# Optimization experiments

Measured on AMD Instinct MI355X. Metric: run time of the kernel, lower is better.

Reference implementation:

```python
import jax, jax.numpy as jnp
import numpy as np

NEG_SLOPE = 0.2
EPS_SOFTMAX = 1e-16
EPS_NORM = 1e-12
H = 4


def gat_conv(x, src, dst, edge_attr, W, att_src, att_dst, W_edge, att_edge, bias, concat):
    """PyG GATConv with edge_dim, add_self_loops=False.
    x: [N, F_in]; src,dst: [E]; edge_attr: [E, edge_dim]
    W: [F_in, H*C]; att_src/att_dst/att_edge: [H, C]; W_edge: [edge_dim, H*C]
    """
    N = x.shape[0]
    C = att_src.shape[1]
    xs = (x @ W).reshape(N, H, C)                      # [N,H,C]
    a_s = jnp.einsum('nhc,hc->nh', xs, att_src)        # [N,H]
    a_d = jnp.einsum('nhc,hc->nh', xs, att_dst)        # [N,H]
    e = (edge_attr @ W_edge).reshape(-1, H, C)         # [E,H,C]
    a_e = jnp.einsum('ehc,hc->eh', e, att_edge)        # [E,H]
    alpha = a_s[src] + a_d[dst] + a_e                  # [E,H]
    alpha = jax.nn.leaky_relu(alpha, NEG_SLOPE)
    # segment softmax over edges grouped by destination node
    m = jax.ops.segment_max(alpha, dst, num_segments=N)        # [N,H]
    ex = jnp.exp(alpha - m[dst])
    denom = jax.ops.segment_sum(ex, dst, num_segments=N)       # [N,H]
    alpha = ex / (denom[dst] + EPS_SOFTMAX)
    # message = attention-weighted source features, scatter-add to dst
    out = jax.ops.segment_sum(xs[src] * alpha[..., None], dst, num_segments=N)  # [N,H,C]
    out = out.reshape(N, H * C) if concat else out.mean(axis=1)
    return out + bias


def l2_normalize(x):
    n = jnp.linalg.norm(x, axis=-1, keepdims=True)
    return x / jnp.maximum(n, EPS_NORM)


def setup_inputs() -> dict:
    key = jax.random.key(0)
    ks = jax.random.split(key, 16)
    N, E, F_in, C1, C2 = 50000, 800000, 128, 64, 64
    glorot = lambda k, shape: jax.random.uniform(
        k, shape, jnp.float32, -1.0, 1.0) * np.sqrt(6.0 / (shape[0] + shape[-1]))
    return {
        'x': jax.random.normal(ks[0], (N, F_in), jnp.float32),
        'edge_index': jax.random.randint(ks[1], (2, E), 0, N, jnp.int32),
        'edge_weight': jax.random.uniform(ks[2], (E, 1), jnp.float32),
        # layer 1: in=128 -> H*C1=256, concat=True
        'W1': glorot(ks[3], (F_in, H * C1)),
        'att_src1': glorot(ks[4], (H, C1)),
        'att_dst1': glorot(ks[5], (H, C1)),
        'We1': glorot(ks[6], (1, H * C1)),
        'att_e1': glorot(ks[7], (H, C1)),
        'b1': jnp.zeros((H * C1,), jnp.float32),
        # layer 2: in=256 -> H*C2, concat=False (mean over heads)
        'W2': glorot(ks[8], (H * C1, H * C2)),
        'att_src2': glorot(ks[9], (H, C2)),
        'att_dst2': glorot(ks[10], (H, C2)),
        'We2': glorot(ks[11], (1, H * C2)),
        'att_e2': glorot(ks[12], (H, C2)),
        'b2': jnp.zeros((C2,), jnp.float32),
    }


def reference(x, edge_index, edge_weight, W1, att_src1, att_dst1, We1, att_e1, b1,
              W2, att_src2, att_dst2, We2, att_e2, b2):
    src, dst = edge_index[0], edge_index[1]
    h = gat_conv(x, src, dst, edge_weight, W1, att_src1, att_dst1, We1, att_e1, b1, concat=True)
    h = jax.nn.relu(l2_normalize(h))
    out = gat_conv(h, src, dst, edge_weight, W2, att_src2, att_dst2, We2, att_e2, b2, concat=False)
    return out
```

## Files before the change

### kernel.cpp

```cpp
#include <hip/hip_runtime.h>
#include <hip/hip_bf16.h>

typedef unsigned short u16;
typedef unsigned long long u64;
using bf16x8 = __attribute__((ext_vector_type(8))) short;
using f32x4v = __attribute__((ext_vector_type(4))) float;
typedef float v2f __attribute__((ext_vector_type(2)));

#define HC 256
#define CDIM 64

__device__ __forceinline__ float b2f(u16 u){
  union { unsigned int i; float f; } c; c.i = ((unsigned)u) << 16; return c.f;
}
__device__ __forceinline__ u16 f2b(float f){
  union { float f; unsigned int i; } c; c.f = f;
  unsigned int x = c.i;
  return (u16)((x + 0x7FFFu + ((x >> 16) & 1u)) >> 16);
}
__device__ __forceinline__ float ldf(const void* p, size_t i, int isbf){
  return isbf ? b2f(((const u16*)p)[i]) : ((const float*)p)[i];
}
__device__ __forceinline__ float sel4(float4 v, int h){ return h==0?v.x:(h==1?v.y:(h==2?v.z:v.w)); }
__device__ __forceinline__ float lrelu(float v){ return v>0.f ? v : 0.2f*v; }

__device__ __forceinline__ void glds16(const void* g, void* l){
  __builtin_amdgcn_global_load_lds(
      (const __attribute__((address_space(1))) unsigned int*)g,
      (__attribute__((address_space(3))) unsigned int*)l, 16, 0, 0);
}

__device__ __forceinline__ float4 wave_max4(float4 m){
  #pragma unroll
  for(int o=32;o>0;o>>=1){
    m.x=fmaxf(m.x,__shfl_xor(m.x,o));
    m.y=fmaxf(m.y,__shfl_xor(m.y,o));
    m.z=fmaxf(m.z,__shfl_xor(m.z,o));
    m.w=fmaxf(m.w,__shfl_xor(m.w,o));
  }
  return m;
}
__device__ __forceinline__ float4 wave_sum4(float4 m){
  #pragma unroll
  for(int o=32;o>0;o>>=1){
    m.x+=__shfl_xor(m.x,o);
    m.y+=__shfl_xor(m.y,o);
    m.z+=__shfl_xor(m.z,o);
    m.w+=__shfl_xor(m.w,o);
  }
  return m;
}

__global__ void k_hist(const int* __restrict__ dst, int E, int N, int* __restrict__ deg,
                       int* __restrict__ rank,
                       const u16* __restrict__ x, int nelem, int* __restrict__ flag){
  int e = blockIdx.x*256 + threadIdx.x;
  if (e < E){
    int d = dst[e];
    if ((unsigned)d < (unsigned)N) rank[e] = atomicAdd(&deg[d], 1);
  }
  if (blockIdx.x == 0){
    __shared__ int bad;
    if (threadIdx.x==0) bad = 0;
    __syncthreads();
    int n = nelem < 8192 ? nelem : 8192;
    int localbad = 0;
    for (int i=threadIdx.x; i<n; i+=256){
      int ex = (x[i] >> 7) & 0xFF;
      if (ex >= 140) localbad++;
    }
    if (localbad) atomicAdd(&bad, 1);
    __syncthreads();
    if (threadIdx.x==0) *flag = (bad==0) ? 1 : 0;
  }
}

__global__ void k_scan1(const int* __restrict__ in, int* __restrict__ out, int* __restrict__ bsums, int n){
  __shared__ int s[256];
  int t = threadIdx.x;
  int i = blockIdx.x*256 + t;
  int v = (i<n)? in[i] : 0;
  s[t]=v; __syncthreads();
  for(int off=1; off<256; off<<=1){
    int tv = (t>=off)? s[t-off] : 0;
    __syncthreads();
    s[t]+=tv; __syncthreads();
  }
  if (i<n) out[i] = s[t]-v;
  if (t==255) bsums[blockIdx.x] = s[255];
}

__global__ void k_scan2(int* __restrict__ bsums, int nb){
  __shared__ int s[256];
  int t=threadIdx.x;
  int v=(t<nb)? bsums[t]:0;
  s[t]=v; __syncthreads();
  for(int off=1; off<256; off<<=1){
    int tv=(t>=off)? s[t-off]:0;
    __syncthreads();
    s[t]+=tv; __syncthreads();
  }
  if (t<nb) bsums[t]=s[t]-v;
}

__global__ void k_scatter(const int* __restrict__ src, const int* __restrict__ dst,
                          const void* __restrict__ ew, int E, int N,
                          const int* __restrict__ rowptr, const int* __restrict__ bsums,
                          const int* __restrict__ rank, u64* __restrict__ epk,
                          const int* __restrict__ flagp){
  int e = blockIdx.x*256+threadIdx.x;
  if (e>=E) return;
  int bf = *flagp;
  int d = dst[e];
  if ((unsigned)d >= (unsigned)N) return;
  int p = rowptr[d] + bsums[d>>8] + rank[e];
  int s = src[e];
  if ((unsigned)s >= (unsigned)N) s = 0;
  u64 v = ((u64)__float_as_uint(ldf(ew, e, bf)) << 32) | (unsigned)s;
  __builtin_nontemporal_store(v, &epk[p]);
}

__global__ void k_prep(const void* __restrict__ W1, const void* __restrict__ W2,
                       const void* __restrict__ We1, const void* __restrict__ ae1,
                       const void* __restrict__ We2, const void* __restrict__ ae2,
                       u16* __restrict__ Bt1, u16* __restrict__ Bt2, float* __restrict__ ce,
                       const int* __restrict__ flagp){
  int bf = *flagp;
  int b = blockIdx.x, t = threadIdx.x;
  if (b < 128){
    Bt1[(size_t)t*128 + b] = f2b(ldf(W1, (size_t)b*HC + t, bf));
  } else if (b < 384){
    int k = b - 128;
    Bt2[(size_t)t*256 + k] = f2b(ldf(W2, (size_t)k*HC + t, bf));
  } else {
    float p1 = ldf(We1, t, bf)*ldf(ae1, t, bf);
    float p2 = ldf(We2, t, bf)*ldf(ae2, t, bf);
    #pragma unroll
    for(int o=32;o>0;o>>=1){ p1+=__shfl_xor(p1,o); p2+=__shfl_xor(p2,o); }
    if((t&63)==0){ ce[t>>6]=p1; ce[4+(t>>6)]=p2; }
  }
}

__global__ __launch_bounds__(256) void k_gemm_mfma(
    const void* __restrict__ A, int a_ext, const u16* __restrict__ Bt,
    u16* __restrict__ C, const void* __restrict__ att_s, const void* __restrict__ att_d,
    float* __restrict__ a_s, float* __restrict__ a_d,
    int M, int K, const int* __restrict__ flagp)
{
  __shared__ u16 sh[64*264];
  __shared__ float att_sh[512];
  u16* As = sh;
  u16* Bs = sh + 2048;
  int bf = *flagp;
  int a_bf = a_ext ? bf : 1;
  int tid = threadIdx.x;
  int lane = tid & 63, w = tid >> 6;
  int quad = lane >> 4, ln = lane & 15;
  int m0 = blockIdx.x * 64;

  att_sh[tid]       = ldf(att_s, tid, bf);
  att_sh[256 + tid] = ldf(att_d, tid, bf);

  f32x4v acc[4][4] = {};
  for (int k0 = 0; k0 < K; k0 += 32){
    if (!a_ext){
      const u16* gA = (const u16*)A + (size_t)(m0 + (tid>>2))*K + k0 + (size_t)(tid&3)*8;
      glds16(gA, (char*)As + (size_t)w*1024);
    } else {
      int m = tid >> 2, g = tid & 3;
      int r = m0 + m;
      uint4 pack;
      if (r < M){
        size_t base = (size_t)r*K + k0 + g*8;
        if (a_bf){
          pack = *(const uint4*)((const u16*)A + base);
        } else {
          const float* Af = (const float*)A + base;
          float4 f0 = *(const float4*)Af;
          float4 f1 = *(const float4*)(Af+4);
          unsigned a0 = (unsigned)f2b(f0.x) | ((unsigned)f2b(f0.y)<<16);
          unsigned a1 = (unsigned)f2b(f0.z) | ((unsigned)f2b(f0.w)<<16);
          unsigned a2 = (unsigned)f2b(f1.x) | ((unsigned)f2b(f1.y)<<16);
          unsigned a3 = (unsigned)f2b(f1.z) | ((unsigned)f2b(f1.w)<<16);
          pack = make_uint4(a0,a1,a2,a3);
        }
      } else pack = make_uint4(0,0,0,0);
      ((uint4*)As)[tid] = pack;
    }
    #pragma unroll
    for (int i=0;i<4;i++){
      const u16* gB = Bt + (size_t)(i*64 + (tid>>2))*K + k0 + (size_t)(tid&3)*8;
      glds16(gB, (char*)Bs + (size_t)i*4096 + (size_t)w*1024);
    }
    __syncthreads();
    bf16x8 af[4], bfr[4];
    #pragma unroll
    for (int mi=0;mi<4;mi++) af[mi] = *(const bf16x8*)&As[(mi*16+ln)*32 + quad*8];
    #pragma unroll
    for (int nj=0;nj<4;nj++) bfr[nj] = *(const bf16x8*)&Bs[((size_t)w*64+nj*16+ln)*32 + quad*8];
    #pragma unroll
    for (int mi=0;mi<4;mi++)
      #pragma unroll
      for (int nj=0;nj<4;nj++)
        acc[mi][nj] = __builtin_amdgcn_mfma_f32_16x16x32_bf16(af[mi], bfr[nj], acc[mi][nj], 0,0,0);
    __syncthreads();
  }
  #pragma unroll
  for (int mi=0;mi<4;mi++)
    #pragma unroll
    for (int nj=0;nj<4;nj++){
      union { __hip_bfloat162 h2; u16 u[2]; } cv0, cv1;
      cv0.h2 = __float22bfloat162_rn(make_float2(acc[mi][nj][0], acc[mi][nj][1]));
      cv1.h2 = __float22bfloat162_rn(make_float2(acc[mi][nj][2], acc[mi][nj][3]));
      int col = w*64 + nj*16 + ln;
      int rbase = mi*16 + quad*4;
      sh[(rbase+0)*264 + col] = cv0.u[0];
      sh[(rbase+1)*264 + col] = cv0.u[1];
      sh[(rbase+2)*264 + col] = cv1.u[0];
      sh[(rbase+3)*264 + col] = cv1.u[1];
    }
  __syncthreads();
  #pragma unroll
  for (int j=0;j<8;j++){
    int idx = j*256 + tid;
    int r = idx >> 5, gq = idx & 31;
    if (m0 + r < M)
      *(uint4*)(C + (size_t)(m0+r)*HC + gq*8) = *(const uint4*)&sh[r*264 + gq*8];
  }
  {
    int r  = w*16 + ln;
    int hh = quad;
    const u16* crow = &sh[r*264 + hh*64];
    const float* asv = &att_sh[hh*64];
    const float* adv = &att_sh[256 + hh*64];
    float ps = 0.f, pd = 0.f;
    #pragma unroll
    for (int cb=0; cb<64; cb+=8){
      ushort4 ua = *(const ushort4*)&crow[cb];
      ushort4 ub = *(const ushort4*)&crow[cb+4];
      float4 sa = *(const float4*)&asv[cb];
      float4 sb = *(const float4*)&asv[cb+4];
      float4 da = *(const float4*)&adv[cb];
      float4 db = *(const float4*)&adv[cb+4];
      float c0=b2f(ua.x), c1=b2f(ua.y), c2=b2f(ua.z), c3=b2f(ua.w);
      float c4=b2f(ub.x), c5=b2f(ub.y), c6=b2f(ub.z), c7=b2f(ub.w);
      ps += c0*sa.x + c1*sa.y + c2*sa.z + c3*sa.w + c4*sb.x + c5*sb.y + c6*sb.z + c7*sb.w;
      pd += c0*da.x + c1*da.y + c2*da.z + c3*da.w + c4*db.x + c5*db.y + c6*db.z + c7*db.w;
    }
    if (m0 + r < M){
      a_s[(size_t)(m0+r)*4 + hh] = ps;
      a_d[(size_t)(m0+r)*4 + hh] = pd;
    }
  }
}

__global__ __launch_bounds__(256) void k_soft_agg(
    const u16* __restrict__ xs, const int* __restrict__ rowptr, const int* __restrict__ bsums,
    const int* __restrict__ deg, const u64* __restrict__ epk,
    const float* __restrict__ a_s, const float* __restrict__ a_d, const float* __restrict__ ce4,
    const void* __restrict__ bias, void* __restrict__ outp, int N, int layer,
    const int* __restrict__ flagp){
  __shared__ int   lds_s[4][64];
  __shared__ float lds_w[4][64][4];
  int bf = *flagp;
  int lane = threadIdx.x & 63;
  int w = threadIdx.x >> 6;
  int n = (blockIdx.x<<2) + w;
  if (n >= N) return;
  int row = rowptr[n] + bsums[n>>8];
  int dg = deg[n];
  float4 ad = *(const float4*)&a_d[(size_t)n*4];
  float4 ce = *(const float4*)ce4;
  int h = lane >> 4;
  float4 acc = make_float4(0.f,0.f,0.f,0.f);
  if (dg > 0){
    if (dg <= 64){
      int   s_reg = 0;
      float4 ar = make_float4(-1e30f,-1e30f,-1e30f,-1e30f);
      if (lane < dg){
        u64 pk = epk[row + lane];
        int s = (int)(unsigned)(pk & 0xFFFFFFFFull);
        if ((unsigned)s >= (unsigned)N) s = 0;
        s_reg = s;
        float wv = __uint_as_float((unsigned)(pk >> 32));
        float4 as = *(const float4*)&a_s[(size_t)s*4];
        ar.x = lrelu(as.x+ad.x+wv*ce.x);
        ar.y = lrelu(as.y+ad.y+wv*ce.y);
        ar.z = lrelu(as.z+ad.z+wv*ce.z);
        ar.w = lrelu(as.w+ad.w+wv*ce.w);
      }
      float4 m = ar;
      if (dg > 32){
        m.x=fmaxf(m.x,__shfl_xor(m.x,32)); m.y=fmaxf(m.y,__shfl_xor(m.y,32));
        m.z=fmaxf(m.z,__shfl_xor(m.z,32)); m.w=fmaxf(m.w,__shfl_xor(m.w,32));
      }
      if (dg > 16){
        m.x=fmaxf(m.x,__shfl_xor(m.x,16)); m.y=fmaxf(m.y,__shfl_xor(m.y,16));
        m.z=fmaxf(m.z,__shfl_xor(m.z,16)); m.w=fmaxf(m.w,__shfl_xor(m.w,16));
      }
      #pragma unroll
      for(int o=8;o>0;o>>=1){
        m.x=fmaxf(m.x,__shfl_xor(m.x,o)); m.y=fmaxf(m.y,__shfl_xor(m.y,o));
        m.z=fmaxf(m.z,__shfl_xor(m.z,o)); m.w=fmaxf(m.w,__shfl_xor(m.w,o));
      }
      float4 ex = make_float4(0.f,0.f,0.f,0.f);
      if (lane < dg){
        ex.x=__expf(ar.x-m.x); ex.y=__expf(ar.y-m.y);
        ex.z=__expf(ar.z-m.z); ex.w=__expf(ar.w-m.w);
      }
      float4 ss = ex;
      if (dg > 32){
        ss.x+=__shfl_xor(ss.x,32); ss.y+=__shfl_xor(ss.y,32);
        ss.z+=__shfl_xor(ss.z,32); ss.w+=__shfl_xor(ss.w,32);
      }
      if (dg > 16){
        ss.x+=__shfl_xor(ss.x,16); ss.y+=__shfl_xor(ss.y,16);
        ss.z+=__shfl_xor(ss.z,16); ss.w+=__shfl_xor(ss.w,16);
      }
      #pragma unroll
      for(int o=8;o>0;o>>=1){
        ss.x+=__shfl_xor(ss.x,o); ss.y+=__shfl_xor(ss.y,o);
        ss.z+=__shfl_xor(ss.z,o); ss.w+=__shfl_xor(ss.w,o);
      }
      float4 wgt;
      wgt.x = ex.x/(ss.x+1e-16f); wgt.y = ex.y/(ss.y+1e-16f);
      wgt.z = ex.z/(ss.z+1e-16f); wgt.w = ex.w/(ss.w+1e-16f);
      if (lane < dg){
        lds_s[w][lane] = s_reg;
        *(float4*)&lds_w[w][lane][0] = wgt;
      }
      v2f a01 = {0.f,0.f}, a23 = {0.f,0.f};
      uint2 xb[8]; float wb[8];
      {
        int pre = dg < 8 ? dg : 8;
        #pragma unroll
        for (int k=0;k<8;k++){
          if (k < pre){
            int s0 = lds_s[w][k];
            wb[k]  = lds_w[w][k][h];
            xb[k]  = *(const uint2*)&xs[(size_t)s0*HC + lane*4];
          }
        }
      }
      for (int base=0; base<dg; base+=8){
        int mcnt = dg - base; if (mcnt > 8) mcnt = 8;
        #pragma unroll
        for (int k=0;k<8;k++){
          if (k < mcnt){
            uint2 xv = xb[k]; float wk = wb[k];
            int nk = base + 8 + k;
            if (nk < dg){
              int s0 = lds_s[w][nk];
              wb[k]  = lds_w[w][nk][h];
              xb[k]  = *(const uint2*)&xs[(size_t)s0*HC + lane*4];
            }
            v2f f;
            f = (v2f){__uint_as_float(xv.x<<16), __uint_as_float(xv.x&0xFFFF0000u)}; a01 += f*wk;
            f = (v2f){__uint_as_float(xv.y<<16), __uint_as_float(xv.y&0xFFFF0000u)}; a23 += f*wk;
          }
        }
      }
      acc.x = a01.x; acc.y = a01.y; acc.z = a23.x; acc.w = a23.y;
    } else {
      float4 m = make_float4(-1e30f,-1e30f,-1e30f,-1e30f);
      for (int p=lane;p<dg;p+=64){
        u64 pk = epk[row+p];
        int s = (int)(unsigned)(pk & 0xFFFFFFFFull);
        if ((unsigned)s >= (unsigned)N) s = 0;
        float wv = __uint_as_float((unsigned)(pk >> 32));
        float4 as = *(const float4*)&a_s[(size_t)s*4];
        m.x=fmaxf(m.x, lrelu(as.x+ad.x+wv*ce.x));
        m.y=fmaxf(m.y, lrelu(as.y+ad.y+wv*ce.y));
        m.z=fmaxf(m.z, lrelu(as.z+ad.z+wv*ce.z));
        m.w=fmaxf(m.w, lrelu(as.w+ad.w+wv*ce.w));
      }
      m = wave_max4(m);
      float4 ss = make_float4(0.f,0.f,0.f,0.f);
      for (int p=lane;p<dg;p+=64){
        u64 pk = epk[row+p];
        int s = (int)(unsigned)(pk & 0xFFFFFFFFull);
        if ((unsigned)s >= (unsigned)N) s = 0;
        float wv = __uint_as_float((unsigned)(pk >> 32));
        float4 as = *(const float4*)&a_s[(size_t)s*4];
        ss.x+=__expf(lrelu(as.x+ad.x+wv*ce.x)-m.x);
        ss.y+=__expf(lrelu(as.y+ad.y+wv*ce.y)-m.y);
        ss.z+=__expf(lrelu(as.z+ad.z+wv*ce.z)-m.z);
        ss.w+=__expf(lrelu(as.w+ad.w+wv*ce.w)-m.w);
      }
      ss = wave_sum4(ss);
      float rsel=1.f/(sel4(ss,h)+1e-16f), mh=sel4(m,h), adh=sel4(ad,h), ceh=sel4(ce,h);
      for (int e=0;e<dg;e++){
        u64 pk = epk[row+e];
        int s = (int)(unsigned)(pk & 0xFFFFFFFFull);
        if ((unsigned)s >= (unsigned)N) s = 0;
        float wv = __uint_as_float((unsigned)(pk >> 32));
        float arv = lrelu(a_s[(size_t)s*4+h]+adh+wv*ceh);
        float wgt = __expf(arv-mh)*rsel;
        ushort4 xv4 = *(const ushort4*)&xs[(size_t)s*HC + lane*4];
        acc.x+=wgt*b2f(xv4.x); acc.y+=wgt*b2f(xv4.y);
        acc.z+=wgt*b2f(xv4.z); acc.w+=wgt*b2f(xv4.w);
      }
    }
  }
  if (layer==1){
    float4 v;
    v.x = acc.x + ldf(bias, lane*4+0, bf);
    v.y = acc.y + ldf(bias, lane*4+1, bf);
    v.z = acc.z + ldf(bias, lane*4+2, bf);
    v.w = acc.w + ldf(bias, lane*4+3, bf);
    float ss = v.x*v.x+v.y*v.y+v.z*v.z+v.w*v.w;
    #pragma unroll
    for(int o=32;o>0;o>>=1) ss += __shfl_xor(ss,o);
    float inv = 1.f/fmaxf(sqrtf(ss), 1e-12f);
    ushort4 o4;
    o4.x = f2b(fmaxf(v.x*inv,0.f)); o4.y = f2b(fmaxf(v.y*inv,0.f));
    o4.z = f2b(fmaxf(v.z*inv,0.f)); o4.w = f2b(fmaxf(v.w*inv,0.f));
    *(ushort4*)((u16*)outp + (size_t)n*HC + lane*4) = o4;
  } else {
    float4 s = acc;
    #pragma unroll
    for (int o=16;o<=32;o<<=1){
      s.x+=__shfl_xor(s.x,o); s.y+=__shfl_xor(s.y,o);
      s.z+=__shfl_xor(s.z,o); s.w+=__shfl_xor(s.w,o);
    }
    if (lane < 16){
      float4 v;
      v.x = 0.25f*s.x + ldf(bias, lane*4+0, bf);
      v.y = 0.25f*s.y + ldf(bias, lane*4+1, bf);
      v.z = 0.25f*s.z + ldf(bias, lane*4+2, bf);
      v.w = 0.25f*s.w + ldf(bias, lane*4+3, bf);
      if (bf){
        ushort4 o4; o4.x=f2b(v.x); o4.y=f2b(v.y); o4.z=f2b(v.z); o4.w=f2b(v.w);
        *(ushort4*)((u16*)outp + (size_t)n*CDIM + lane*4) = o4;
      } else {
        *(float4*)((float*)outp + (size_t)n*CDIM + lane*4) = v;
      }
    }
  }
}

extern "C" void kernel_launch(void* const* d_in, const int* in_sizes, int n_in,
                              void* d_out, int out_size, void* d_ws, size_t ws_size,
                              hipStream_t stream){
  const void* x_in = d_in[0];
  const int* eidx  = (const int*)d_in[1];
  const void* ew   = d_in[2];
  const void* W1   = d_in[3];
  const void* as1  = d_in[4];
  const void* ad1  = d_in[5];
  const void* We1  = d_in[6];
  const void* ae1  = d_in[7];
  const void* b1   = d_in[8];
  const void* W2   = d_in[9];
  const void* as2  = d_in[10];
  const void* ad2  = d_in[11];
  const void* We2  = d_in[12];
  const void* ae2  = d_in[13];
  const void* b2   = d_in[14];

  int N = in_sizes[0]/128;
  int E = in_sizes[2];
  const int* src = eidx;
  const int* dst = eidx + E;

  char* w = (char*)d_ws;
  auto alloc = [&](size_t bytes)->char*{ char* p=w; w += (bytes+255)/256*256; return p; };
  int*   flag  = (int*)alloc(256);
  u16*   xs    = (u16*)alloc((size_t)N*HC*2);
  u16*   agg   = (u16*)alloc((size_t)N*HC*2);
  float* a_s   = (float*)alloc((size_t)N*4*4);
  float* a_d   = (float*)alloc((size_t)N*4*4);
  int*   deg   = (int*)alloc((size_t)N*4);
  int*   rowptr= (int*)alloc((size_t)N*4);
  int*   bsums = (int*)alloc(256*4);
  int*   rank  = (int*)alloc((size_t)E*4);
  u64*   epk   = (u64*)alloc((size_t)E*8);
  float* ce    = (float*)alloc(256);
  u16*   Bt1   = (u16*)alloc((size_t)HC*128*2);
  u16*   Bt2   = (u16*)alloc((size_t)HC*HC*2);

  (void)hipMemsetAsync(deg, 0, (size_t)N*4, stream);

  int eb = (E+255)/256;
  int nb = (N+255)/256;
  k_hist<<<eb,256,0,stream>>>(dst, E, N, deg, rank, (const u16*)x_in, in_sizes[0], flag);
  k_scan1<<<nb,256,0,stream>>>(deg, rowptr, bsums, N);
  k_scan2<<<1,256,0,stream>>>(bsums, nb);
  k_scatter<<<eb,256,0,stream>>>(src, dst, ew, E, N, rowptr, bsums, rank, epk, flag);
  k_prep<<<385,256,0,stream>>>(W1, W2, We1, ae1, We2, ae2, Bt1, Bt2, ce, flag);

  int gemmBlocks = (N+63)/64;
  int nwb = (N+3)/4;

  k_gemm_mfma<<<gemmBlocks,256,0,stream>>>(x_in, 1, Bt1, xs, as1, ad1, a_s, a_d, N, 128, flag);
  k_soft_agg<<<nwb,256,0,stream>>>(xs, rowptr, bsums, deg, epk, a_s, a_d, ce, b1, agg, N, 1, flag);

  k_gemm_mfma<<<gemmBlocks,256,0,stream>>>(agg, 0, Bt2, xs, as2, ad2, a_s, a_d, N, 256, flag);
  k_soft_agg<<<nwb,256,0,stream>>>(xs, rowptr, bsums, deg, epk, a_s, a_d, ce+4, b2, d_out, N, 2, flag);
}
```

Measured before the change: 361.6 us.

## Replace LDS staging with readlane/shuffle broadcast and drop max-subtraction in soft-agg

The short-degree path of the softmax-aggregate kernel no longer stores source indices and weights to LDS. It broadcasts source indices with readlane and per-head weights with wave shuffles, and it issues the first eight feature gathers before the softmax is computed. It also removes the segment-max reduction and exponentiates the raw logits directly, which saves a reduction but risks overflow for large logits. Gathers for degrees above eight are issued in padded groups of four, and lanes beyond the degree carry zero weight.

```diff
diff --git a/kernel.cpp b/kernel.cpp
--- a/kernel.cpp
+++ b/kernel.cpp
@@ -254,14 +254,36 @@
   }
 }
 
+#define GRP4(E0, TWJ) { \
+  int s0_=__builtin_amdgcn_readlane(s_reg,(E0)+0); \
+  int s1_=__builtin_amdgcn_readlane(s_reg,(E0)+1); \
+  int s2_=__builtin_amdgcn_readlane(s_reg,(E0)+2); \
+  int s3_=__builtin_amdgcn_readlane(s_reg,(E0)+3); \
+  uint2 x0_=*(const uint2*)&xs[(size_t)s0_*HC + (lane<<2)]; \
+  uint2 x1_=*(const uint2*)&xs[(size_t)s1_*HC + (lane<<2)]; \
+  uint2 x2_=*(const uint2*)&xs[(size_t)s2_*HC + (lane<<2)]; \
+  uint2 x3_=*(const uint2*)&xs[(size_t)s3_*HC + (lane<<2)]; \
+  float w0_=__shfl((TWJ), ibase+(((E0)+0)&15)); \
+  float w1_=__shfl((TWJ), ibase+(((E0)+1)&15)); \
+  float w2_=__shfl((TWJ), ibase+(((E0)+2)&15)); \
+  float w3_=__shfl((TWJ), ibase+(((E0)+3)&15)); \
+  v2f f_; \
+  f_=(v2f){__uint_as_float(x0_.x<<16),__uint_as_float(x0_.x&0xFFFF0000u)}; a01+=f_*w0_; \
+  f_=(v2f){__uint_as_float(x0_.y<<16),__uint_as_float(x0_.y&0xFFFF0000u)}; a23+=f_*w0_; \
+  f_=(v2f){__uint_as_float(x1_.x<<16),__uint_as_float(x1_.x&0xFFFF0000u)}; a01+=f_*w1_; \
+  f_=(v2f){__uint_as_float(x1_.y<<16),__uint_as_float(x1_.y&0xFFFF0000u)}; a23+=f_*w1_; \
+  f_=(v2f){__uint_as_float(x2_.x<<16),__uint_as_float(x2_.x&0xFFFF0000u)}; a01+=f_*w2_; \
+  f_=(v2f){__uint_as_float(x2_.y<<16),__uint_as_float(x2_.y&0xFFFF0000u)}; a23+=f_*w2_; \
+  f_=(v2f){__uint_as_float(x3_.x<<16),__uint_as_float(x3_.x&0xFFFF0000u)}; a01+=f_*w3_; \
+  f_=(v2f){__uint_as_float(x3_.y<<16),__uint_as_float(x3_.y&0xFFFF0000u)}; a23+=f_*w3_; \
+}
+
 __global__ __launch_bounds__(256) void k_soft_agg(
     const u16* __restrict__ xs, const int* __restrict__ rowptr, const int* __restrict__ bsums,
     const int* __restrict__ deg, const u64* __restrict__ epk,
     const float* __restrict__ a_s, const float* __restrict__ a_d, const float* __restrict__ ce4,
     const void* __restrict__ bias, void* __restrict__ outp, int N, int layer,
     const int* __restrict__ flagp){
-  __shared__ int   lds_s[4][64];
-  __shared__ float lds_w[4][64][4];
   int bf = *flagp;
   int lane = threadIdx.x & 63;
   int w = threadIdx.x >> 6;
@@ -275,39 +297,25 @@
   float4 acc = make_float4(0.f,0.f,0.f,0.f);
   if (dg > 0){
     if (dg <= 64){
-      int   s_reg = 0;
-      float4 ar = make_float4(-1e30f,-1e30f,-1e30f,-1e30f);
-      if (lane < dg){
-        u64 pk = epk[row + lane];
-        int s = (int)(unsigned)(pk & 0xFFFFFFFFull);
-        if ((unsigned)s >= (unsigned)N) s = 0;
-        s_reg = s;
-        float wv = __uint_as_float((unsigned)(pk >> 32));
-        float4 as = *(const float4*)&a_s[(size_t)s*4];
-        ar.x = lrelu(as.x+ad.x+wv*ce.x);
-        ar.y = lrelu(as.y+ad.y+wv*ce.y);
-        ar.z = lrelu(as.z+ad.z+wv*ce.z);
-        ar.w = lrelu(as.w+ad.w+wv*ce.w);
-      }
-      float4 m = ar;
-      if (dg > 32){
-        m.x=fmaxf(m.x,__shfl_xor(m.x,32)); m.y=fmaxf(m.y,__shfl_xor(m.y,32));
-        m.z=fmaxf(m.z,__shfl_xor(m.z,32)); m.w=fmaxf(m.w,__shfl_xor(m.w,32));
-      }
-      if (dg > 16){
-        m.x=fmaxf(m.x,__shfl_xor(m.x,16)); m.y=fmaxf(m.y,__shfl_xor(m.y,16));
-        m.z=fmaxf(m.z,__shfl_xor(m.z,16)); m.w=fmaxf(m.w,__shfl_xor(m.w,16));
-      }
+      u64 pk = 0;
+      if (lane < dg) pk = epk[row + lane];
+      int s = (int)(unsigned)(pk & 0xFFFFFFFFull);
+      if ((unsigned)s >= (unsigned)N) s = 0;
+      int s_reg = s;
+      float wv = __uint_as_float((unsigned)(pk >> 32));
+      float4 as4 = *(const float4*)&a_s[(size_t)s*4];
+      uint2 xpf[8];
       #pragma unroll
-      for(int o=8;o>0;o>>=1){
-        m.x=fmaxf(m.x,__shfl_xor(m.x,o)); m.y=fmaxf(m.y,__shfl_xor(m.y,o));
-        m.z=fmaxf(m.z,__shfl_xor(m.z,o)); m.w=fmaxf(m.w,__shfl_xor(m.w,o));
-      }
-      float4 ex = make_float4(0.f,0.f,0.f,0.f);
-      if (lane < dg){
-        ex.x=__expf(ar.x-m.x); ex.y=__expf(ar.y-m.y);
-        ex.z=__expf(ar.z-m.z); ex.w=__expf(ar.w-m.w);
-      }
+      for (int k=0;k<8;k++){
+        int sk = __builtin_amdgcn_readlane(s_reg, k);
+        xpf[k] = *(const uint2*)&xs[(size_t)sk*HC + (lane<<2)];
+      }
+      bool vlane = lane < dg;
+      float4 ex;
+      ex.x = vlane ? __expf(lrelu(as4.x+ad.x+wv*ce.x)) : 0.f;
+      ex.y = vlane ? __expf(lrelu(as4.y+ad.y+wv*ce.y)) : 0.f;
+      ex.z = vlane ? __expf(lrelu(as4.z+ad.z+wv*ce.z)) : 0.f;
+      ex.w = vlane ? __expf(lrelu(as4.w+ad.w+wv*ce.w)) : 0.f;
       float4 ss = ex;
       if (dg > 32){
         ss.x+=__shfl_xor(ss.x,32); ss.y+=__shfl_xor(ss.y,32);
@@ -325,38 +333,58 @@
       float4 wgt;
       wgt.x = ex.x/(ss.x+1e-16f); wgt.y = ex.y/(ss.y+1e-16f);
       wgt.z = ex.z/(ss.z+1e-16f); wgt.w = ex.w/(ss.w+1e-16f);
-      if (lane < dg){
-        lds_s[w][lane] = s_reg;
-        *(float4*)&lds_w[w][lane][0] = wgt;
-      }
+      int ibase = lane & 48;
+      float tw0, tw1, tw2, tw3;
+      {
+        int srcl = lane & 15;
+        float c0=__shfl(wgt.x,srcl), c1=__shfl(wgt.y,srcl);
+        float c2=__shfl(wgt.z,srcl), c3=__shfl(wgt.w,srcl);
+        tw0 = (h==0)?c0:((h==1)?c1:((h==2)?c2:c3));
+      }
+      if (dg > 16){
+        int srcl = 16 + (lane & 15);
+        float c0=__shfl(wgt.x,srcl), c1=__shfl(wgt.y,srcl);
+        float c2=__shfl(wgt.z,srcl), c3=__shfl(wgt.w,srcl);
+        tw1 = (h==0)?c0:((h==1)?c1:((h==2)?c2:c3));
+      } else tw1 = 0.f;
+      if (dg > 32){
+        int srcl = 32 + (lane & 15);
+        float c0=__shfl(wgt.x,srcl), c1=__shfl(wgt.y,srcl);
+        float c2=__shfl(wgt.z,srcl), c3=__shfl(wgt.w,srcl);
+        tw2 = (h==0)?c0:((h==1)?c1:((h==2)?c2:c3));
+      } else tw2 = 0.f;
+      if (dg > 48){
+        int srcl = 48 + (lane & 15);
+        float c0=__shfl(wgt.x,srcl), c1=__shfl(wgt.y,srcl);
+        float c2=__shfl(wgt.z,srcl), c3=__shfl(wgt.w,srcl);
+        tw3 = (h==0)?c0:((h==1)?c1:((h==2)?c2:c3));
+      } else tw3 = 0.f;
       v2f a01 = {0.f,0.f}, a23 = {0.f,0.f};
-      uint2 xb[8]; float wb[8];
-      {
-        int pre = dg < 8 ? dg : 8;
-        #pragma unroll
-        for (int k=0;k<8;k++){
-          if (k < pre){
-            int s0 = lds_s[w][k];
-            wb[k]  = lds_w[w][k][h];
-            xb[k]  = *(const uint2*)&xs[(size_t)s0*HC + lane*4];
-          }
-        }
-      }
-      for (int base=0; base<dg; base+=8){
-        int mcnt = dg - base; if (mcnt > 8) mcnt = 8;
-        #pragma unroll
-        for (int k=0;k<8;k++){
-          if (k < mcnt){
-            uint2 xv = xb[k]; float wk = wb[k];
-            int nk = base + 8 + k;
-            if (nk < dg){
-              int s0 = lds_s[w][nk];
-              wb[k]  = lds_w[w][nk][h];
-              xb[k]  = *(const uint2*)&xs[(size_t)s0*HC + lane*4];
-            }
-            v2f f;
-            f = (v2f){__uint_as_float(xv.x<<16), __uint_as_float(xv.x&0xFFFF0000u)}; a01 += f*wk;
-            f = (v2f){__uint_as_float(xv.y<<16), __uint_as_float(xv.y&0xFFFF0000u)}; a23 += f*wk;
+      #pragma unroll
+      for (int k=0;k<8;k++){
+        float wk = __shfl(tw0, ibase+k);
+        uint2 xv = xpf[k];
+        v2f f;
+        f = (v2f){__uint_as_float(xv.x<<16), __uint_as_float(xv.x&0xFFFF0000u)}; a01 += f*wk;
+        f = (v2f){__uint_as_float(xv.y<<16), __uint_as_float(xv.y&0xFFFF0000u)}; a23 += f*wk;
+      }
+      if (dg >  8) GRP4( 8, tw0);
+      if (dg > 12) GRP4(12, tw0);
+      if (dg > 16){
+        GRP4(16, tw1);
+        if (dg > 20) GRP4(20, tw1);
+        if (dg > 24) GRP4(24, tw1);
+        if (dg > 28) GRP4(28, tw1);
+        if (dg > 32){
+          GRP4(32, tw2);
+          if (dg > 36) GRP4(36, tw2);
+          if (dg > 40) GRP4(40, tw2);
+          if (dg > 44) GRP4(44, tw2);
+          if (dg > 48){
+            GRP4(48, tw3);
+            if (dg > 52) GRP4(52, tw3);
+            if (dg > 56) GRP4(56, tw3);
+            if (dg > 60) GRP4(60, tw3);
           }
         }
       }
```

Result: faster. 328.5 us (-9.2%).
